# Performance work log

Hardware: AMD Instinct MI355X
Metric: run time of the kernel (lower is better)

The kernel has to match this reference:

```python
import jax, jax.numpy as jnp
import numpy as np

N_AUTHOR, N_PAPER = 20000, 40000
E = 400000
IN_DIM, HIDDEN, HEADS, NUM_CLASSES, NUM_LAYERS = 128, 128, 8, 16, 2
DIM = HIDDEN // HEADS
NEG_SLOPE = 0.2
AUTHOR_RAW = 64


def setup_inputs() -> dict:
    key = jax.random.key(0)
    ks = jax.random.split(key, 16)
    s = 0.05
    return {
        'x_author': jax.random.normal(ks[0], (N_AUTHOR, AUTHOR_RAW), jnp.float32),
        'x_paper': jax.random.normal(ks[1], (N_PAPER, IN_DIM), jnp.float32),
        'Wa': jax.random.normal(ks[2], (AUTHOR_RAW, IN_DIM), jnp.float32) * s,
        'proj_w': jax.random.normal(ks[3], (NUM_LAYERS, 2, IN_DIM, HIDDEN), jnp.float32) * s,
        'proj_b': jnp.zeros((NUM_LAYERS, 2, HIDDEN), jnp.float32),
        'att_src': jax.random.normal(ks[4], (NUM_LAYERS, 3, HEADS, DIM), jnp.float32) * s,
        'att_dst': jax.random.normal(ks[5], (NUM_LAYERS, 3, HEADS, DIM), jnp.float32) * s,
        'klin_w': jax.random.normal(ks[6], (NUM_LAYERS, HIDDEN, HIDDEN), jnp.float32) * s,
        'klin_b': jnp.zeros((NUM_LAYERS, HIDDEN), jnp.float32),
        'q': jax.random.normal(ks[7], (NUM_LAYERS, HIDDEN), jnp.float32) * s,
        'lin_w': jax.random.normal(ks[8], (HIDDEN, NUM_CLASSES), jnp.float32) * s,
        'lin_b': jnp.zeros((NUM_CLASSES,), jnp.float32),
        'ei_writes': jnp.stack([jax.random.randint(ks[9], (E,), 0, N_AUTHOR),
                                jax.random.randint(ks[10], (E,), 0, N_PAPER)]),
        'ei_written_by': jnp.stack([jax.random.randint(ks[11], (E,), 0, N_PAPER),
                                    jax.random.randint(ks[12], (E,), 0, N_AUTHOR)]),
        'ei_cites': jnp.stack([jax.random.randint(ks[13], (E,), 0, N_PAPER),
                               jax.random.randint(ks[14], (E,), 0, N_PAPER)]),
    }


def _segment_softmax(scores, seg, num_segments):
    # scores: [E, H]; softmax over edges sharing a destination node.
    m = jax.ops.segment_max(scores, seg, num_segments=num_segments)
    m = jnp.where(jnp.isfinite(m), m, 0.0)
    e = jnp.exp(scores - m[seg])
    denom = jax.ops.segment_sum(e, seg, num_segments=num_segments)
    return e / (denom[seg] + 1e-16)


def _han_forward(x_author, x_paper, Wa, proj_w, proj_b, att_src, att_dst,
                 klin_w, klin_b, q, lin_w, lin_b,
                 ei_writes, ei_written_by, ei_cites):
    # Type-alignment projector (author: 64 -> 128, no bias; paper: Identity)
    x = {'author': x_author @ Wa, 'paper': x_paper}
    nsize = {'author': N_AUTHOR, 'paper': N_PAPER}
    ntidx = {'author': 0, 'paper': 1}
    edge_types = [('author', 'paper', ei_writes),
                  ('paper', 'author', ei_written_by),
                  ('paper', 'paper', ei_cites)]
    for l in range(NUM_LAYERS):
        # Per-node-type projection -> [N, H, D]
        xh = {nt: (x[nt] @ proj_w[l, ntidx[nt]] + proj_b[l, ntidx[nt]]).reshape(-1, HEADS, DIM)
              for nt in x}
        outs = {'author': [], 'paper': []}
        for e_id, (src, dst, ei) in enumerate(edge_types):
            a_src = (xh[src] * att_src[l, e_id]).sum(-1)  # [N_src, H]
            a_dst = (xh[dst] * att_dst[l, e_id]).sum(-1)  # [N_dst, H]
            si, di = ei[0], ei[1]
            alpha = a_src[si] + a_dst[di]                 # [E, H]
            alpha = jnp.where(alpha >= 0, alpha, NEG_SLOPE * alpha)  # leaky_relu
            alpha = _segment_softmax(alpha, di, nsize[dst])
            # attention dropout omitted (eval mode)
            msg = (xh[src][si] * alpha[:, :, None]).reshape(-1, HIDDEN)  # [E, HIDDEN]
            agg = jax.ops.segment_sum(msg, di, num_segments=nsize[dst])
            outs[dst].append(jax.nn.relu(agg))
        # Semantic-level attention over metapath embeddings per node type
        newx = {}
        for nt, xs in outs.items():
            stk = jnp.stack(xs)  # [M, N, F]
            score = (q[l] * jnp.tanh(stk @ klin_w[l] + klin_b[l]).mean(axis=1)).sum(-1)  # [M]
            attn = jax.nn.softmax(score)
            newx[nt] = (attn[:, None, None] * stk).sum(0)
        x = newx
        if l < NUM_LAYERS - 1:
            x = {nt: jax.nn.relu(v) for nt, v in x.items()}
            # feature dropout omitted (eval mode)
    return x['paper'] @ lin_w + lin_b  # [N_PAPER, NUM_CLASSES]


def reference(x_author, x_paper, Wa, proj_w, proj_b, att_src, att_dst,
              klin_w, klin_b, q, lin_w, lin_b,
              ei_writes, ei_written_by, ei_cites):
    return _han_forward(x_author, x_paper, Wa, proj_w, proj_b, att_src, att_dst,
                        klin_w, klin_b, q, lin_w, lin_b,
                        ei_writes, ei_written_by, ei_cites)
```

## Files before the change

### kernel.cpp

```cpp
#include <hip/hip_runtime.h>
#include <hip/hip_bf16.h>

typedef __hip_bfloat16 bf16;
typedef __hip_bfloat162 bf162;

#define N_AUTHOR 20000
#define N_PAPER  40000
#define NEDGE    400000
#define HID      128
#define HEADS    8
#define DIMH     16
#define NCLS     16

typedef short short8v __attribute__((ext_vector_type(8)));
typedef float f32x4   __attribute__((ext_vector_type(4)));

__device__ __forceinline__ float b2f(short s){
    return __uint_as_float(((unsigned)(unsigned short)s) << 16);
}
__device__ __forceinline__ short f2bs(float v){
    unsigned u = __float_as_uint(v);
    unsigned r = (u + 0x7FFFu + ((u >> 16) & 1u)) >> 16;
    return (short)r;
}
__device__ __forceinline__ float fastrcp(float x){ return __builtin_amdgcn_rcpf(x); }

__device__ __forceinline__ float fast_tanh(float x){
    x = fminf(fmaxf(x, -15.f), 15.f);
    float e = __expf(2.f * x);
    return 1.f - 2.f * fastrcp(e + 1.f);
}

template<int KDIM, int EPI, int BLEND, int AF32>
__device__ __forceinline__ void bgemm_body(
    const void* __restrict__ Av, const bf16* __restrict__ A2, float w0, float w1,
    const bf16* __restrict__ Wt, const float* __restrict__ Bb,
    bf16* __restrict__ C, const float* __restrict__ qv, float* __restrict__ score,
    int M, int brow, float* red)
{
    const int tid  = threadIdx.x;
    const int lane = tid & 63;
    const int wv   = tid >> 6;
    const int lr   = lane & 15;
    const int quad = lane >> 4;
    const int row0 = brow * 64 + wv * 16;
    const int arow_i = row0 + lr;
    const bool rowok = arow_i < M;

    short8v afrag[KDIM / 32];
    if (AF32) {
        const float* arow = (const float*)Av + (long)arow_i * KDIM;
        #pragma unroll
        for (int kc = 0; kc < KDIM / 32; kc++) {
            short8v f = {0,0,0,0,0,0,0,0};
            if (rowok) {
                float4 v0 = *(const float4*)(arow + kc * 32 + quad * 8);
                float4 v1 = *(const float4*)(arow + kc * 32 + quad * 8 + 4);
                f[0] = f2bs(v0.x); f[1] = f2bs(v0.y); f[2] = f2bs(v0.z); f[3] = f2bs(v0.w);
                f[4] = f2bs(v1.x); f[5] = f2bs(v1.y); f[6] = f2bs(v1.z); f[7] = f2bs(v1.w);
            }
            afrag[kc] = f;
        }
    } else {
        const bf16* arow  = (const bf16*)Av + (long)arow_i * KDIM;
        const bf16* arow2 = BLEND ? (A2 + (long)arow_i * KDIM) : nullptr;
        #pragma unroll
        for (int kc = 0; kc < KDIM / 32; kc++) {
            short8v f = {0,0,0,0,0,0,0,0};
            if (rowok) {
                f = *(const short8v*)(arow + kc * 32 + quad * 8);
                if (BLEND) {
                    short8v g = *(const short8v*)(arow2 + kc * 32 + quad * 8);
                    #pragma unroll
                    for (int j = 0; j < 8; j++)
                        f[j] = f2bs(w0 * b2f(f[j]) + w1 * b2f(g[j]));
                }
            }
            afrag[kc] = f;
        }
    }

    f32x4 acc[8];
    #pragma unroll
    for (int ct = 0; ct < 8; ct++) acc[ct] = (f32x4){0.f, 0.f, 0.f, 0.f};

    #pragma unroll
    for (int k0 = 0; k0 < KDIM / 32; k0 += 2) {
        short8v bf[2][8];
        #pragma unroll
        for (int u = 0; u < 2; u++)
            #pragma unroll
            for (int ct = 0; ct < 8; ct++)
                bf[u][ct] = *(const short8v*)(Wt + (long)(ct * 16 + lr) * KDIM + (k0 + u) * 32 + quad * 8);
        #pragma unroll
        for (int u = 0; u < 2; u++)
            #pragma unroll
            for (int ct = 0; ct < 8; ct++)
                acc[ct] = __builtin_amdgcn_mfma_f32_16x16x32_bf16(afrag[k0 + u], bf[u][ct], acc[ct], 0, 0, 0);
    }

    if (EPI == 0) {
        #pragma unroll
        for (int ct = 0; ct < 8; ct++) {
            float bc = Bb ? Bb[ct * 16 + lr] : 0.f;
            #pragma unroll
            for (int r = 0; r < 4; r++) {
                int orow = row0 + quad * 4 + r;
                if (orow < M)
                    C[(long)orow * HID + ct * 16 + lr] = __float2bfloat16(acc[ct][r] + bc);
            }
        }
    } else {
        float part = 0.f;
        #pragma unroll
        for (int ct = 0; ct < 8; ct++) {
            float bc = Bb ? Bb[ct * 16 + lr] : 0.f;
            float qc = qv[ct * 16 + lr];
            #pragma unroll
            for (int r = 0; r < 4; r++) {
                int orow = row0 + quad * 4 + r;
                if (orow < M) part += qc * fast_tanh(acc[ct][r] + bc);
            }
        }
        red[tid] = part;
        __syncthreads();
        for (int s = 128; s > 0; s >>= 1) {
            if (tid < s) red[tid] += red[tid + s];
            __syncthreads();
        }
        if (tid == 0) atomicAdd(score, red[0]);
    }
}

template<int KDIM, int EPI, int B1>
__global__ __launch_bounds__(256) void bgemm_pair_kernel(
    const bf16* __restrict__ A0, const bf16* __restrict__ Wt0, const float* __restrict__ Bb0,
    bf16* __restrict__ C0, float* __restrict__ score0, int M0, int NB0,
    const bf16* __restrict__ A1, const bf16* __restrict__ A1b, const float* __restrict__ scw,
    const bf16* __restrict__ Wt1, const float* __restrict__ Bb1,
    bf16* __restrict__ C1, float* __restrict__ score1, int M1,
    const float* __restrict__ qv)
{
    __shared__ float red[256];
    const int bx = blockIdx.x;
    if (bx < NB0) {
        bgemm_body<KDIM, EPI, 0, 0>(A0, nullptr, 0.f, 0.f, Wt0, Bb0, C0, qv, score0, M0, bx, red);
    } else {
        float w0 = 0.f, w1 = 0.f;
        if (B1) {
            float s0 = scw[0] * (1.f / N_PAPER);
            float s1 = scw[1] * (1.f / N_PAPER);
            float m = fmaxf(s0, s1);
            float e0 = __expf(s0 - m), e1 = __expf(s1 - m);
            float inv = fastrcp(e0 + e1);
            w0 = e0 * inv; w1 = e1 * inv;
        }
        bgemm_body<KDIM, EPI, B1, 0>(A1, A1b, w0, w1, Wt1, Bb1, C1, qv, score1, M1, bx - NB0, red);
    }
}

#define R_WA  (128 * 64)
#define R_PW  (4 * 128 * 128)
#define R_KW  (2 * 128 * 128)
#define CONV_W_TOT (R_WA + R_PW + R_KW)

#define CNT_OFF1 N_PAPER
#define CNT_OFF2 (N_PAPER + N_AUTHOR)
#define NDEST    (2 * N_PAPER + N_AUTHOR)
#define NCOPY 8
#define CW    2
#define CIDX(c, d) (((c) * NDEST + (d)) * CW)
#define CNT_TOT (NCOPY * NDEST * CW)
#define E3 (3 * NEDGE)
#define HU 16
#define HIST_TT (E3 / HU)

__global__ __launch_bounds__(256) void convw_kernel(
    const float* __restrict__ Wa, const float* __restrict__ proj_w,
    const float* __restrict__ klin_w,
    bf16* __restrict__ wt_wa, bf16* __restrict__ wt_proj, bf16* __restrict__ wt_klin)
{
    int i = blockIdx.x * 256 + threadIdx.x;
    if (i >= CONV_W_TOT) return;
    if (i < R_WA) {
        int n = i >> 6, k = i & 63;
        wt_wa[i] = __float2bfloat16(Wa[k * 128 + n]);
    } else if (i < R_WA + R_PW) {
        int j = i - R_WA;
        int m = j >> 14, r = j & 16383;
        int n = r >> 7, k = r & 127;
        wt_proj[j] = __float2bfloat16(proj_w[m * 16384 + k * 128 + n]);
    } else {
        int j = i - R_WA - R_PW;
        int m = j >> 14, r = j & 16383;
        int n = r >> 7, k = r & 127;
        wt_klin[j] = __float2bfloat16(klin_w[m * 16384 + k * 128 + n]);
    }
}

__global__ __launch_bounds__(256) void hist_gemm_kernel(
    const int* __restrict__ d0, const int* __restrict__ d1, const int* __restrict__ d2,
    int* __restrict__ cnt, unsigned short* __restrict__ rank, int HB,
    const float* __restrict__ xa_f, const bf16* __restrict__ wt_wa, bf16* __restrict__ buf_a, int GA64,
    const float* __restrict__ xp_f, const bf16* __restrict__ pw_p, const float* __restrict__ pb_p,
    bf16* __restrict__ xh_p)
{
    __shared__ float red[256];
    int bx = blockIdx.x;
    if (bx < HB) {
        int c = bx & (NCOPY - 1);
        int* mycnt = cnt + c * NDEST * CW;
        int t = bx * 256 + threadIdx.x;
        if (t >= HIST_TT) return;
        #pragma unroll
        for (int u = 0; u < HU; u++) {
            int i = t + u * HIST_TT;
            int r;
            if (i < NEDGE)            r = atomicAdd(&mycnt[d0[i] * CW], 1);
            else if (i < 2*NEDGE)     r = atomicAdd(&mycnt[(CNT_OFF1 + d1[i - NEDGE]) * CW], 1);
            else                      r = atomicAdd(&mycnt[(CNT_OFF2 + d2[i - 2*NEDGE]) * CW], 1);
            rank[i] = (unsigned short)((c << 13) | r);
        }
        return;
    }
    bx -= HB;
    if (bx < GA64) {
        bgemm_body<64, 0, 0, 1>(xa_f, nullptr, 0.f, 0.f, wt_wa, nullptr, buf_a,
                                nullptr, nullptr, N_AUTHOR, bx, red);
        return;
    }
    bx -= GA64;
    bgemm_body<128, 0, 0, 1>(xp_f, nullptr, 0.f, 0.f, pw_p, pb_p, xh_p,
                             nullptr, nullptr, N_PAPER, bx, red);
}

__device__ __forceinline__ int job_nd(int j){ return j == 1 ? N_AUTHOR : N_PAPER; }
__device__ __forceinline__ int job_off(int j){ return j == 0 ? 0 : (j == 1 ? CNT_OFF1 : CNT_OFF2); }

__global__ __launch_bounds__(256) void scan_a3_kernel(const int* __restrict__ cnt,
                                                      int* __restrict__ bsum)
{
    int j = blockIdx.y;
    int nd = job_nd(j), off = job_off(j);
    __shared__ int s[256];
    int tid = threadIdx.x;
    int i = blockIdx.x * 256 + tid;
    int v = 0;
    if (i < nd) {
        #pragma unroll
        for (int c = 0; c < NCOPY; c++) v += cnt[CIDX(c, off + i)];
    }
    s[tid] = v;
    __syncthreads();
    for (int st = 128; st > 0; st >>= 1) {
        if (tid < st) s[tid] += s[tid + st];
        __syncthreads();
    }
    if (tid == 0) bsum[j * 256 + blockIdx.x] = s[0];
}

__global__ __launch_bounds__(256) void scan_bc_kernel(int* __restrict__ cnt,
    const int* __restrict__ bsum,
    int* __restrict__ roff0, int* __restrict__ roff1, int* __restrict__ roff2)
{
    int j = blockIdx.y;
    int nd = job_nd(j), off = job_off(j);
    int* roff = j == 0 ? roff0 : (j == 1 ? roff1 : roff2);
    __shared__ int sb[256];
    __shared__ int s[256];
    int tid = threadIdx.x;
    int bx = blockIdx.x;
    int nb = (nd + 255) / 256;
    int bvt = (tid < nb) ? bsum[j * 256 + tid] : 0;
    sb[tid] = bvt;
    __syncthreads();
    for (int o = 1; o < 256; o <<= 1) {
        int t = (tid >= o) ? sb[tid - o] : 0;
        __syncthreads();
        sb[tid] += t;
        __syncthreads();
    }
    int base0 = sb[bx] - bsum[j * 256 + bx];
    int i = bx * 256 + tid;
    int cc[NCOPY];
    int v = 0;
    if (i < nd) {
        #pragma unroll
        for (int c = 0; c < NCOPY; c++) { cc[c] = cnt[CIDX(c, off + i)]; v += cc[c]; }
    }
    s[tid] = v;
    __syncthreads();
    for (int o = 1; o < 256; o <<= 1) {
        int t = (tid >= o) ? s[tid - o] : 0;
        __syncthreads();
        s[tid] += t;
        __syncthreads();
    }
    if (i < nd) {
        int base = base0 + s[tid] - v;
        roff[i] = base;
        #pragma unroll
        for (int c = 0; c < NCOPY; c++) { cnt[CIDX(c, off + i)] = base; base += cc[c]; }
    }
    if (bx == 0 && tid == 0) roff[nd] = NEDGE;
}

__global__ __launch_bounds__(256) void fill_natt_kernel(
    const int* __restrict__ s0, const int* __restrict__ d0,
    const int* __restrict__ s1, const int* __restrict__ d1,
    const int* __restrict__ s2, const int* __restrict__ d2,
    const int* __restrict__ cnt, const unsigned short* __restrict__ rank,
    unsigned short* __restrict__ c0, unsigned short* __restrict__ c1, unsigned short* __restrict__ c2,
    int HB,
    const bf16* __restrict__ A, const bf16* __restrict__ Wt, const float* __restrict__ Bb,
    bf16* __restrict__ C, int GAb,
    const bf16* __restrict__ xh_p,
    const float* __restrict__ ad0v, const float* __restrict__ as1v,
    const float* __restrict__ as2v, const float* __restrict__ ad2v,
    float* __restrict__ o_e0d, float* __restrict__ o_e1s,
    float* __restrict__ o_e2s, float* __restrict__ o_e2d)
{
    __shared__ float red[256];
    int bx = blockIdx.x;
    if (bx < HB) {
        int t = bx * 256 + threadIdx.x;
        if (t >= HIST_TT) return;
        #pragma unroll
        for (int u = 0; u < HU; u++) {
            int i = t + u * HIST_TT;
            int rw = rank[i];
            int c = rw >> 13, rk = rw & 0x1FFF;
            if (i < NEDGE) {
                int d = d0[i];
                c0[cnt[CIDX(c, d)] + rk] = (unsigned short)s0[i];
            } else if (i < 2*NEDGE) {
                int e = i - NEDGE, d = d1[e];
                c1[cnt[CIDX(c, CNT_OFF1 + d)] + rk] = (unsigned short)s1[e];
            } else {
                int e = i - 2*NEDGE, d = d2[e];
                c2[cnt[CIDX(c, CNT_OFF2 + d)] + rk] = (unsigned short)s2[e];
            }
        }
        return;
    }
    bx -= HB;
    if (bx < GAb) {
        bgemm_body<128, 0, 0, 0>(A, nullptr, 0.f, 0.f, Wt, Bb, C,
                                 nullptr, nullptr, N_AUTHOR, bx, red);
        return;
    }
    bx -= GAb;
    int i = bx * 256 + threadIdx.x;
    if (i >= N_PAPER * HEADS) return;
    int n = i >> 3, h = i & 7;
    const bf16* row = xh_p + (long)n * HID + h * DIMH;
    float x[DIMH];
    #pragma unroll
    for (int d = 0; d < DIMH; d++) x[d] = __bfloat162float(row[d]);
    float sA = 0.f, sB = 0.f, sC = 0.f, sD = 0.f;
    #pragma unroll
    for (int d = 0; d < DIMH; d++) {
        sA += x[d] * ad0v[h*DIMH + d];
        sB += x[d] * as1v[h*DIMH + d];
        sC += x[d] * as2v[h*DIMH + d];
        sD += x[d] * ad2v[h*DIMH + d];
    }
    o_e0d[i] = sA; o_e1s[i] = sB; o_e2s[i] = sC; o_e2d[i] = sD;
}

__global__ void node_att_multi_kernel(const bf16* __restrict__ xh,
    const float* __restrict__ A0, const float* __restrict__ A1,
    float* __restrict__ O0, float* __restrict__ O1, int N)
{
    int i = blockIdx.x * blockDim.x + threadIdx.x;
    if (i >= N * HEADS) return;
    int n = i >> 3, h = i & 7;
    const bf16* row = xh + (long)n * HID + h * DIMH;
    float x[DIMH];
    #pragma unroll
    for (int d = 0; d < DIMH; d++) x[d] = __bfloat162float(row[d]);
    if (A0) { float s = 0.f;
        #pragma unroll
        for (int d = 0; d < DIMH; d++) s += x[d] * A0[h*DIMH + d];
        O0[i] = s; }
    if (A1) { float s = 0.f;
        #pragma unroll
        for (int d = 0; d < DIMH; d++) s += x[d] * A1[h*DIMH + d];
        O1[i] = s; }
}

__global__ __launch_bounds__(256) void natt_l1_kernel(
    const bf16* __restrict__ xh_a, const float* __restrict__ as0, float* __restrict__ a_e0s, int AB,
    const bf16* __restrict__ xh_p, const float* __restrict__ ad0,
    const float* __restrict__ as2, const float* __restrict__ ad2,
    float* __restrict__ a_e0d, float* __restrict__ a_e2s, float* __restrict__ a_e2d)
{
    int bx = blockIdx.x, tid = threadIdx.x;
    if (bx < AB) {
        int i = bx * 256 + tid;
        if (i >= N_AUTHOR * HEADS) return;
        int n = i >> 3, h = i & 7;
        const bf16* row = xh_a + (long)n * HID + h * DIMH;
        float s = 0.f;
        #pragma unroll
        for (int d = 0; d < DIMH; d++) s += __bfloat162float(row[d]) * as0[h*DIMH + d];
        a_e0s[i] = s;
        return;
    }
    int i = (bx - AB) * 256 + tid;
    if (i >= N_PAPER * HEADS) return;
    int n = i >> 3, h = i & 7;
    const bf16* row = xh_p + (long)n * HID + h * DIMH;
    float x[DIMH];
    #pragma unroll
    for (int d = 0; d < DIMH; d++) x[d] = __bfloat162float(row[d]);
    float sA = 0.f, sC = 0.f, sD = 0.f;
    #pragma unroll
    for (int d = 0; d < DIMH; d++) {
        sA += x[d] * ad0[h*DIMH + d];
        sC += x[d] * as2[h*DIMH + d];
        sD += x[d] * ad2[h*DIMH + d];
    }
    a_e0d[i] = sA; a_e2s[i] = sC; a_e2d[i] = sD;
}

template<int U>
__device__ __forceinline__ void gather1_dev(int bid,
    const int* __restrict__ roff, const unsigned short* __restrict__ csrc,
    const float* __restrict__ as_, const float* __restrict__ ad_,
    const bf16* __restrict__ xh, bf16* __restrict__ out, int Ndst)
{
    int lane = threadIdx.x & 63;
    int li   = lane & 15;
    int sub  = lane >> 4;
    int w = bid * 16 + (threadIdx.x >> 6) * 4 + sub;
    if (w >= Ndst) return;
    int h = li >> 1;
    int beg = roff[w], n = roff[w + 1] - beg;
    float adv = ad_[(long)w * 8 + h];
    float den = 0.f;
    float acc[8];
    #pragma unroll
    for (int j = 0; j < 8; j++) acc[j] = 0.f;
    int cm = n > 0 ? n - 1 : 0;
    for (int i = 0; i < n; i += U) {
        int s[U];
        #pragma unroll
        for (int u = 0; u < U; u++) s[u] = csrc[beg + min(i + u, cm)];
        float av[U]; short8v xv[U];
        #pragma unroll
        for (int u = 0; u < U; u++) {
            av[u] = as_[(long)s[u] * 8 + h];
            xv[u] = *(const short8v*)(xh + (long)s[u] * HID + li * 8);
        }
        #pragma unroll
        for (int u = 0; u < U; u++) {
            float a = av[u] + adv;
            a = a >= 0.f ? a : 0.2f * a;
            float wt = __expf(fminf(a, 60.f));
            wt = (i + u < n) ? wt : 0.f;
            den += wt;
            #pragma unroll
            for (int j = 0; j < 8; j++)
                acc[j] = fmaf(b2f(xv[u][j]), wt, acc[j]);
        }
    }
    float inv = fastrcp(den + 1e-16f);
    short8v o;
    #pragma unroll
    for (int j = 0; j < 8; j++) o[j] = f2bs(fmaxf(acc[j] * inv, 0.f));
    *(short8v*)(out + (long)w * HID + li * 8) = o;
}

__global__ __launch_bounds__(256) void gather_split_kernel(
    const int* __restrict__ roff0, const unsigned short* __restrict__ csrc0,
    const float* __restrict__ as0, const float* __restrict__ ad0,
    const bf16* __restrict__ xha, bf16* __restrict__ out0,
    const int* __restrict__ roff2, const unsigned short* __restrict__ csrc2,
    const float* __restrict__ as2, const float* __restrict__ ad2,
    const bf16* __restrict__ xhp, bf16* __restrict__ out2,
    int PB,
    const int* __restrict__ roff1, const unsigned short* __restrict__ csrc1,
    const float* __restrict__ as1, const float* __restrict__ ad1,
    bf16* __restrict__ out_a)
{
    int bx = blockIdx.x;
    if (bx < PB) {
        gather1_dev<8>(bx, roff0, csrc0, as0, ad0, xha, out0, N_PAPER);
        return;
    }
    bx -= PB;
    if (bx < PB) {
        gather1_dev<8>(bx, roff2, csrc2, as2, ad2, xhp, out2, N_PAPER);
        return;
    }
    bx -= PB;
    gather1_dev<8>(bx, roff1, csrc1, as1, ad1, xhp, out_a, N_AUTHOR);
}

__global__ __launch_bounds__(256) void final_lin_fused_kernel(
    const bf16* __restrict__ a0, const bf16* __restrict__ a1,
    const float* __restrict__ score,
    const float* __restrict__ W, const float* __restrict__ B, float* __restrict__ out)
{
    __shared__ float Ws[HID * NCLS];
    int tid = threadIdx.x;
    for (int i = tid; i < HID * NCLS; i += 256) Ws[i] = W[i];
    __syncthreads();
    float s0 = score[0] * (1.f / N_PAPER);
    float s1 = score[1] * (1.f / N_PAPER);
    float m = fmaxf(s0, s1);
    float e0 = __expf(s0 - m), e1 = __expf(s1 - m);
    float inv = 1.f / (e0 + e1);
    float w0 = e0 * inv, w1 = e1 * inv;
    int i = blockIdx.x * 256 + tid;
    if (i >= N_PAPER * NCLS) return;
    int n = i >> 4, c = i & 15;
    float acc = B[c];
    const bf16* x0 = a0 + (long)n * HID;
    const bf16* x1 = a1 + (long)n * HID;
    #pragma unroll 16
    for (int k = 0; k < HID; k++)
        acc = fmaf(fmaf(w0, __bfloat162float(x0[k]), w1 * __bfloat162float(x1[k])),
                   Ws[k * NCLS + c], acc);
    out[i] = acc;
}

extern "C" void kernel_launch(void* const* d_in, const int* in_sizes, int n_in,
                              void* d_out, int out_size, void* d_ws, size_t ws_size,
                              hipStream_t stream)
{
    const float* x_author = (const float*)d_in[0];
    const float* x_paper  = (const float*)d_in[1];
    const float* Wa       = (const float*)d_in[2];
    const float* proj_w   = (const float*)d_in[3];
    const float* proj_b   = (const float*)d_in[4];
    const float* att_src  = (const float*)d_in[5];
    const float* att_dst  = (const float*)d_in[6];
    const float* klin_w   = (const float*)d_in[7];
    const float* klin_b   = (const float*)d_in[8];
    const float* qv       = (const float*)d_in[9];
    const float* lin_w    = (const float*)d_in[10];
    const float* lin_b    = (const float*)d_in[11];
    const int*  ei_w      = (const int*)d_in[12];
    const int*  ei_wb     = (const int*)d_in[13];
    const int*  ei_c      = (const int*)d_in[14];
    float* out = (float*)d_out;
    (void)ws_size; (void)in_sizes; (void)n_in; (void)out_size;

    char* base = (char*)d_ws;
    size_t off = 0;
    auto alloc = [&](size_t bytes) {
        void* p = base + off;
        off = (off + bytes + 255) & ~(size_t)255;
        return p;
    };
    bf16*  xh_a  = (bf16*) alloc((size_t)N_AUTHOR * HID * 2);
    bf16*  xh_p  = (bf16*) alloc((size_t)N_PAPER  * HID * 2);
    bf16*  buf_a = (bf16*) alloc((size_t)N_AUTHOR * HID * 2);
    bf16*  buf_p = (bf16*) alloc((size_t)N_PAPER  * HID * 2);
    bf16*  agg_p1= (bf16*) alloc((size_t)N_PAPER  * HID * 2);
    bf16*  wt_wa   = (bf16*)alloc((size_t)R_WA * 2);
    bf16*  wt_proj = (bf16*)alloc((size_t)R_PW * 2);
    bf16*  wt_klin = (bf16*)alloc((size_t)R_KW * 2);
    float* a_e0s = (float*)alloc((size_t)N_AUTHOR * HEADS * 4);
    float* a_e0d = (float*)alloc((size_t)N_PAPER  * HEADS * 4);
    float* a_e1s = (float*)alloc((size_t)N_PAPER  * HEADS * 4);
    float* a_e1d = (float*)alloc((size_t)N_AUTHOR * HEADS * 4);
    float* a_e2s = (float*)alloc((size_t)N_PAPER  * HEADS * 4);
    float* a_e2d = (float*)alloc((size_t)N_PAPER  * HEADS * 4);
    float* score  = (float*)alloc(64);
    int* roff0 = (int*)alloc((size_t)(N_PAPER  + 1) * 4);
    int* roff1 = (int*)alloc((size_t)(N_AUTHOR + 1) * 4);
    int* roff2 = (int*)alloc((size_t)(N_PAPER  + 1) * 4);
    unsigned short* csrc0 = (unsigned short*)alloc((size_t)NEDGE * 2 + 64);
    unsigned short* csrc1 = (unsigned short*)alloc((size_t)NEDGE * 2 + 64);
    unsigned short* csrc2 = (unsigned short*)alloc((size_t)NEDGE * 2 + 64);
    int* cnt   = (int*)alloc((size_t)CNT_TOT * 4);
    unsigned short* rank = (unsigned short*)alloc((size_t)E3 * 2);
    int* bsum  = (int*)alloc(3 * 256 * 4);

    const int GA = (N_AUTHOR + 63) / 64;
    const int GP = (N_PAPER  + 63) / 64;
    const int NBMAX = (N_PAPER + 255) / 256;
    const int HB = (HIST_TT + 255) / 256;
    const int CONVB = (CONV_W_TOT + 255) / 256;
    const int NATTP = (N_PAPER * HEADS + 255) / 256;
    const int NATTA = (N_AUTHOR * HEADS + 255) / 256;
    const int PGB = (N_PAPER + 15) / 16;
    const int AGB = (N_AUTHOR + 15) / 16;

    hipMemsetAsync(cnt, 0, (size_t)CNT_TOT * 4, stream);
    hipMemsetAsync(score, 0, 64, stream);

    convw_kernel<<<CONVB, 256, 0, stream>>>(
        Wa, proj_w, klin_w, wt_wa, wt_proj, wt_klin);
    hist_gemm_kernel<<<HB + GA + GP, 256, 0, stream>>>(
        ei_w + NEDGE, ei_wb + NEDGE, ei_c + NEDGE, cnt, rank, HB,
        x_author, wt_wa, buf_a, GA,
        x_paper, wt_proj + (size_t)1 * HID * HID, proj_b + (size_t)1 * HID, xh_p);
    scan_a3_kernel<<<dim3(NBMAX, 3), 256, 0, stream>>>(cnt, bsum);
    scan_bc_kernel<<<dim3(NBMAX, 3), 256, 0, stream>>>(cnt, bsum, roff0, roff1, roff2);

    const float* as0_0 = att_src + 0 * HID; const float* ad0_0 = att_dst + 0 * HID;
    const float* as1_0 = att_src + 1 * HID; const float* ad1_0 = att_dst + 1 * HID;
    const float* as2_0 = att_src + 2 * HID; const float* ad2_0 = att_dst + 2 * HID;

    fill_natt_kernel<<<HB + GA + NATTP, 256, 0, stream>>>(
        ei_w, ei_w + NEDGE, ei_wb, ei_wb + NEDGE, ei_c, ei_c + NEDGE,
        cnt, rank, csrc0, csrc1, csrc2, HB,
        buf_a, wt_proj + (size_t)0 * HID * HID, proj_b + (size_t)0 * HID, xh_a, GA,
        xh_p, ad0_0, as1_0, as2_0, ad2_0,
        a_e0d, a_e1s, a_e2s, a_e2d);
    node_att_multi_kernel<<<NATTA, 256, 0, stream>>>(
        xh_a, as0_0, ad1_0, a_e0s, a_e1d, N_AUTHOR);

    gather_split_kernel<<<2 * PGB + AGB, 256, 0, stream>>>(
        roff0, csrc0, a_e0s, a_e0d, xh_a, buf_p,
        roff2, csrc2, a_e2s, a_e2d, xh_p, agg_p1,
        PGB,
        roff1, csrc1, a_e1s, a_e1d, buf_a);

    bgemm_pair_kernel<128, 1, 0><<<2 * GP, 256, 0, stream>>>(
        buf_p, wt_klin, klin_b, (bf16*)nullptr, score + 0, N_PAPER, GP,
        agg_p1, nullptr, nullptr, wt_klin, klin_b, (bf16*)nullptr, score + 1, N_PAPER,
        qv);

    bgemm_pair_kernel<128, 0, 1><<<GA + GP, 256, 0, stream>>>(
        buf_a, wt_proj + (size_t)2 * HID * HID, proj_b + (size_t)2 * HID, xh_a,
        nullptr, N_AUTHOR, GA,
        buf_p, agg_p1, score,
        wt_proj + (size_t)3 * HID * HID, proj_b + (size_t)3 * HID, xh_p,
        nullptr, N_PAPER, nullptr);
    hipMemsetAsync(score, 0, 64, stream);

    const float* as0_1 = att_src + 3 * HID; const float* ad0_1 = att_dst + 3 * HID;
    const float* as2_1 = att_src + 5 * HID; const float* ad2_1 = att_dst + 5 * HID;

    natt_l1_kernel<<<NATTA + NATTP, 256, 0, stream>>>(
        xh_a, as0_1, a_e0s, NATTA,
        xh_p, ad0_1, as2_1, ad2_1, a_e0d, a_e2s, a_e2d);

    gather_split_kernel<<<2 * PGB, 256, 0, stream>>>(
        roff0, csrc0, a_e0s, a_e0d, xh_a, buf_p,
        roff2, csrc2, a_e2s, a_e2d, xh_p, agg_p1,
        PGB,
        roff1, csrc1, a_e1s, a_e1d, nullptr);

    bgemm_pair_kernel<128, 1, 0><<<2 * GP, 256, 0, stream>>>(
        buf_p, wt_klin + (size_t)HID * HID, klin_b + HID, (bf16*)nullptr, score + 0, N_PAPER, GP,
        agg_p1, nullptr, nullptr, wt_klin + (size_t)HID * HID, klin_b + HID,
        (bf16*)nullptr, score + 1, N_PAPER,
        qv + HID);

    final_lin_fused_kernel<<<(N_PAPER * NCLS + 255) / 256, 256, 0, stream>>>(
        buf_p, agg_p1, score, lin_w, lin_b, out);
}
```

Baseline: 397.1 us.

## Replace global atomic histogram with LDS-partitioned per-copy histograms

The destination-count histogram now runs in shared memory. Each block owns one of 8 edge chunks and one 8192-wide destination range, scans the whole chunk, does LDS atomics for in-range destinations, then writes its counts to global memory. This removes the global atomics, the padded count stride and the memset of the count array. In exchange, each edge index is read 13 times across the partitions, the block count is fixed at 104 per histogram, and the GEMM blocks share a larger 32 KB LDS allocation, which may reduce their occupancy.

```diff
diff --git a/kernel.cpp b/kernel.cpp
--- a/kernel.cpp
+++ b/kernel.cpp
@@ -168,12 +168,16 @@
 #define CNT_OFF2 (N_PAPER + N_AUTHOR)
 #define NDEST    (2 * N_PAPER + N_AUTHOR)
 #define NCOPY 8
-#define CW    2
-#define CIDX(c, d) (((c) * NDEST + (d)) * CW)
-#define CNT_TOT (NCOPY * NDEST * CW)
+#define CIDX(c, d) ((c) * NDEST + (d))
+#define CNT_TOT (NCOPY * NDEST)
 #define E3 (3 * NEDGE)
 #define HU 16
 #define HIST_TT (E3 / HU)
+
+#define PART_SZ 8192
+#define NPART   13
+#define CHUNK   (E3 / NCOPY)
+#define HBLK    (NPART * NCOPY)
 
 __global__ __launch_bounds__(256) void convw_kernel(
     const float* __restrict__ Wa, const float* __restrict__ proj_w,
@@ -200,38 +204,61 @@
 
 __global__ __launch_bounds__(256) void hist_gemm_kernel(
     const int* __restrict__ d0, const int* __restrict__ d1, const int* __restrict__ d2,
-    int* __restrict__ cnt, unsigned short* __restrict__ rank, int HB,
+    int* __restrict__ cnt, unsigned short* __restrict__ rank,
     const float* __restrict__ xa_f, const bf16* __restrict__ wt_wa, bf16* __restrict__ buf_a, int GA64,
     const float* __restrict__ xp_f, const bf16* __restrict__ pw_p, const float* __restrict__ pb_p,
     bf16* __restrict__ xh_p)
 {
-    __shared__ float red[256];
+    __shared__ int lh[PART_SZ];
     int bx = blockIdx.x;
-    if (bx < HB) {
-        int c = bx & (NCOPY - 1);
-        int* mycnt = cnt + c * NDEST * CW;
-        int t = bx * 256 + threadIdx.x;
-        if (t >= HIST_TT) return;
-        #pragma unroll
-        for (int u = 0; u < HU; u++) {
-            int i = t + u * HIST_TT;
-            int r;
-            if (i < NEDGE)            r = atomicAdd(&mycnt[d0[i] * CW], 1);
-            else if (i < 2*NEDGE)     r = atomicAdd(&mycnt[(CNT_OFF1 + d1[i - NEDGE]) * CW], 1);
-            else                      r = atomicAdd(&mycnt[(CNT_OFF2 + d2[i - 2*NEDGE]) * CW], 1);
-            rank[i] = (unsigned short)((c << 13) | r);
+    int tid = threadIdx.x;
+    if (bx < HBLK) {
+        int p = bx % NPART;
+        int c = bx / NPART;
+        #pragma unroll
+        for (int k = tid; k < PART_SZ; k += 256) lh[k] = 0;
+        __syncthreads();
+        const int base = c * CHUNK;
+        const int lo = p * PART_SZ;
+        for (int k0 = 0; k0 < CHUNK; k0 += 2048) {
+            int dd[8];
+            #pragma unroll
+            for (int u = 0; u < 8; u++) {
+                int k = k0 + u * 256 + tid;
+                int dglob = -1;
+                if (k < CHUNK) {
+                    int i = base + k;
+                    if (i < NEDGE)          dglob = d0[i];
+                    else if (i < 2*NEDGE)   dglob = CNT_OFF1 + d1[i - NEDGE];
+                    else                    dglob = CNT_OFF2 + d2[i - 2*NEDGE];
+                }
+                dd[u] = dglob;
+            }
+            #pragma unroll
+            for (int u = 0; u < 8; u++) {
+                int ld = dd[u] - lo;
+                if (dd[u] >= 0 && ld >= 0 && ld < PART_SZ) {
+                    int r = atomicAdd(&lh[ld], 1);
+                    rank[base + k0 + u * 256 + tid] = (unsigned short)((c << 13) | r);
+                }
+            }
+        }
+        __syncthreads();
+        for (int ld = tid; ld < PART_SZ; ld += 256) {
+            int d = lo + ld;
+            if (d < NDEST) cnt[CIDX(c, d)] = lh[ld];
         }
         return;
     }
-    bx -= HB;
+    bx -= HBLK;
     if (bx < GA64) {
         bgemm_body<64, 0, 0, 1>(xa_f, nullptr, 0.f, 0.f, wt_wa, nullptr, buf_a,
-                                nullptr, nullptr, N_AUTHOR, bx, red);
+                                nullptr, nullptr, N_AUTHOR, bx, (float*)lh);
         return;
     }
     bx -= GA64;
     bgemm_body<128, 0, 0, 1>(xp_f, nullptr, 0.f, 0.f, pw_p, pb_p, xh_p,
-                             nullptr, nullptr, N_PAPER, bx, red);
+                             nullptr, nullptr, N_PAPER, bx, (float*)lh);
 }
 
 __device__ __forceinline__ int job_nd(int j){ return j == 1 ? N_AUTHOR : N_PAPER; }
@@ -590,13 +617,12 @@
     const int PGB = (N_PAPER + 15) / 16;
     const int AGB = (N_AUTHOR + 15) / 16;
 
-    hipMemsetAsync(cnt, 0, (size_t)CNT_TOT * 4, stream);
     hipMemsetAsync(score, 0, 64, stream);
 
     convw_kernel<<<CONVB, 256, 0, stream>>>(
         Wa, proj_w, klin_w, wt_wa, wt_proj, wt_klin);
-    hist_gemm_kernel<<<HB + GA + GP, 256, 0, stream>>>(
-        ei_w + NEDGE, ei_wb + NEDGE, ei_c + NEDGE, cnt, rank, HB,
+    hist_gemm_kernel<<<HBLK + GA + GP, 256, 0, stream>>>(
+        ei_w + NEDGE, ei_wb + NEDGE, ei_c + NEDGE, cnt, rank,
         x_author, wt_wa, buf_a, GA,
         x_paper, wt_proj + (size_t)1 * HID * HID, proj_b + (size_t)1 * HID, xh_p);
     scan_a3_kernel<<<dim3(NBMAX, 3), 256, 0, stream>>>(cnt, bsum);
```

Measured after the change: 573.2 us. +44.3%, slower.

## Fuse node attention dot products into projection GEMM epilogues and regroup launches

Applied to the files above, without the earlier changes.

Computes the per-head attention source/destination scores directly in the projection GEMM epilogue from the fp32 accumulators, using cross-lane shuffles over 16 columns. This removes the separate node-attention kernels, which re-read the bf16 projected features. Launches are regrouped: the author projection for layer 1 now runs alongside the semantic klin GEMMs in one mid kernel, and the paper projection gets its own kernel. The trade-off is extra shuffle work and scattered 4-byte stores in the GEMM epilogue, and the attention scores now come from unrounded fp32 values rather than bf16.

```diff
diff --git a/kernel.cpp b/kernel.cpp
--- a/kernel.cpp
+++ b/kernel.cpp
@@ -31,12 +31,16 @@
     return 1.f - 2.f * fastrcp(e + 1.f);
 }
 
-template<int KDIM, int EPI, int BLEND, int AF32>
+template<int KDIM, int EPI, int BLEND, int AF32, int NATT>
 __device__ __forceinline__ void bgemm_body(
     const void* __restrict__ Av, const bf16* __restrict__ A2, float w0, float w1,
     const bf16* __restrict__ Wt, const float* __restrict__ Bb,
     bf16* __restrict__ C, const float* __restrict__ qv, float* __restrict__ score,
-    int M, int brow, float* red)
+    int M, int brow, float* red,
+    const float* __restrict__ at0, const float* __restrict__ at1,
+    const float* __restrict__ at2, const float* __restrict__ at3,
+    float* __restrict__ o0, float* __restrict__ o1,
+    float* __restrict__ o2, float* __restrict__ o3)
 {
     const int tid  = threadIdx.x;
     const int lane = tid & 63;
@@ -103,11 +107,35 @@
         #pragma unroll
         for (int ct = 0; ct < 8; ct++) {
             float bc = Bb ? Bb[ct * 16 + lr] : 0.f;
+            float av0 = (NATT > 0) ? at0[ct * 16 + lr] : 0.f;
+            float av1 = (NATT > 1) ? at1[ct * 16 + lr] : 0.f;
+            float av2 = (NATT > 2) ? at2[ct * 16 + lr] : 0.f;
+            float av3 = (NATT > 3) ? at3[ct * 16 + lr] : 0.f;
             #pragma unroll
             for (int r = 0; r < 4; r++) {
                 int orow = row0 + quad * 4 + r;
+                float cb = acc[ct][r] + bc;
                 if (orow < M)
-                    C[(long)orow * HID + ct * 16 + lr] = __float2bfloat16(acc[ct][r] + bc);
+                    C[(long)orow * HID + ct * 16 + lr] = __float2bfloat16(cb);
+                if (NATT > 0) {
+                    float d0 = cb * av0;
+                    float d1 = cb * av1;
+                    float d2 = cb * av2;
+                    float d3 = cb * av3;
+                    #pragma unroll
+                    for (int mm = 1; mm < 16; mm <<= 1) {
+                        d0 += __shfl_xor(d0, mm);
+                        if (NATT > 1) d1 += __shfl_xor(d1, mm);
+                        if (NATT > 2) d2 += __shfl_xor(d2, mm);
+                        if (NATT > 3) d3 += __shfl_xor(d3, mm);
+                    }
+                    if (lr == 0 && orow < M) {
+                        o0[(long)orow * 8 + ct] = d0;
+                        if (NATT > 1) o1[(long)orow * 8 + ct] = d1;
+                        if (NATT > 2) o2[(long)orow * 8 + ct] = d2;
+                        if (NATT > 3) o3[(long)orow * 8 + ct] = d3;
+                    }
+                }
             }
         }
     } else {
@@ -129,33 +157,6 @@
             __syncthreads();
         }
         if (tid == 0) atomicAdd(score, red[0]);
-    }
-}
-
-template<int KDIM, int EPI, int B1>
-__global__ __launch_bounds__(256) void bgemm_pair_kernel(
-    const bf16* __restrict__ A0, const bf16* __restrict__ Wt0, const float* __restrict__ Bb0,
-    bf16* __restrict__ C0, float* __restrict__ score0, int M0, int NB0,
-    const bf16* __restrict__ A1, const bf16* __restrict__ A1b, const float* __restrict__ scw,
-    const bf16* __restrict__ Wt1, const float* __restrict__ Bb1,
-    bf16* __restrict__ C1, float* __restrict__ score1, int M1,
-    const float* __restrict__ qv)
-{
-    __shared__ float red[256];
-    const int bx = blockIdx.x;
-    if (bx < NB0) {
-        bgemm_body<KDIM, EPI, 0, 0>(A0, nullptr, 0.f, 0.f, Wt0, Bb0, C0, qv, score0, M0, bx, red);
-    } else {
-        float w0 = 0.f, w1 = 0.f;
-        if (B1) {
-            float s0 = scw[0] * (1.f / N_PAPER);
-            float s1 = scw[1] * (1.f / N_PAPER);
-            float m = fmaxf(s0, s1);
-            float e0 = __expf(s0 - m), e1 = __expf(s1 - m);
-            float inv = fastrcp(e0 + e1);
-            w0 = e0 * inv; w1 = e1 * inv;
-        }
-        bgemm_body<KDIM, EPI, B1, 0>(A1, A1b, w0, w1, Wt1, Bb1, C1, qv, score1, M1, bx - NB0, red);
     }
 }
 
@@ -203,7 +204,11 @@
     int* __restrict__ cnt, unsigned short* __restrict__ rank, int HB,
     const float* __restrict__ xa_f, const bf16* __restrict__ wt_wa, bf16* __restrict__ buf_a, int GA64,
     const float* __restrict__ xp_f, const bf16* __restrict__ pw_p, const float* __restrict__ pb_p,
-    bf16* __restrict__ xh_p)
+    bf16* __restrict__ xh_p,
+    const float* __restrict__ ad0v, const float* __restrict__ as1v,
+    const float* __restrict__ as2v, const float* __restrict__ ad2v,
+    float* __restrict__ a_e0d, float* __restrict__ a_e1s,
+    float* __restrict__ a_e2s, float* __restrict__ a_e2d)
 {
     __shared__ float red[256];
     int bx = blockIdx.x;
@@ -225,13 +230,17 @@
     }
     bx -= HB;
     if (bx < GA64) {
-        bgemm_body<64, 0, 0, 1>(xa_f, nullptr, 0.f, 0.f, wt_wa, nullptr, buf_a,
-                                nullptr, nullptr, N_AUTHOR, bx, red);
+        bgemm_body<64, 0, 0, 1, 0>(xa_f, nullptr, 0.f, 0.f, wt_wa, nullptr, buf_a,
+                                   nullptr, nullptr, N_AUTHOR, bx, red,
+                                   nullptr, nullptr, nullptr, nullptr,
+                                   nullptr, nullptr, nullptr, nullptr);
         return;
     }
     bx -= GA64;
-    bgemm_body<128, 0, 0, 1>(xp_f, nullptr, 0.f, 0.f, pw_p, pb_p, xh_p,
-                             nullptr, nullptr, N_PAPER, bx, red);
+    bgemm_body<128, 0, 0, 1, 4>(xp_f, nullptr, 0.f, 0.f, pw_p, pb_p, xh_p,
+                                nullptr, nullptr, N_PAPER, bx, red,
+                                ad0v, as1v, as2v, ad2v,
+                                a_e0d, a_e1s, a_e2s, a_e2d);
 }
 
 __device__ __forceinline__ int job_nd(int j){ return j == 1 ? N_AUTHOR : N_PAPER; }
@@ -305,7 +314,7 @@
     if (bx == 0 && tid == 0) roff[nd] = NEDGE;
 }
 
-__global__ __launch_bounds__(256) void fill_natt_kernel(
+__global__ __launch_bounds__(256) void fill_gemm_kernel(
     const int* __restrict__ s0, const int* __restrict__ d0,
     const int* __restrict__ s1, const int* __restrict__ d1,
     const int* __restrict__ s2, const int* __restrict__ d2,
@@ -313,12 +322,9 @@
     unsigned short* __restrict__ c0, unsigned short* __restrict__ c1, unsigned short* __restrict__ c2,
     int HB,
     const bf16* __restrict__ A, const bf16* __restrict__ Wt, const float* __restrict__ Bb,
-    bf16* __restrict__ C, int GAb,
-    const bf16* __restrict__ xh_p,
-    const float* __restrict__ ad0v, const float* __restrict__ as1v,
-    const float* __restrict__ as2v, const float* __restrict__ ad2v,
-    float* __restrict__ o_e0d, float* __restrict__ o_e1s,
-    float* __restrict__ o_e2s, float* __restrict__ o_e2d)
+    bf16* __restrict__ C,
+    const float* __restrict__ as0v, const float* __restrict__ ad1v,
+    float* __restrict__ a_e0s, float* __restrict__ a_e1d)
 {
     __shared__ float red[256];
     int bx = blockIdx.x;
@@ -344,84 +350,82 @@
         return;
     }
     bx -= HB;
-    if (bx < GAb) {
-        bgemm_body<128, 0, 0, 0>(A, nullptr, 0.f, 0.f, Wt, Bb, C,
-                                 nullptr, nullptr, N_AUTHOR, bx, red);
+    bgemm_body<128, 0, 0, 0, 2>(A, nullptr, 0.f, 0.f, Wt, Bb, C,
+                                nullptr, nullptr, N_AUTHOR, bx, red,
+                                as0v, ad1v, nullptr, nullptr,
+                                a_e0s, a_e1d, nullptr, nullptr);
+}
+
+__global__ __launch_bounds__(256) void mid_kernel(
+    const bf16* __restrict__ buf_p, const bf16* __restrict__ agg_p1,
+    const bf16* __restrict__ kw, const float* __restrict__ kb,
+    float* __restrict__ score, const float* __restrict__ qq, int GP_,
+    const bf16* __restrict__ buf_a, const bf16* __restrict__ pw_a, const float* __restrict__ pb_a,
+    bf16* __restrict__ xh_a,
+    const float* __restrict__ as0v, float* __restrict__ a_e0s)
+{
+    __shared__ float red[256];
+    int bx = blockIdx.x;
+    if (bx < GP_) {
+        bgemm_body<128, 1, 0, 0, 0>(buf_p, nullptr, 0.f, 0.f, kw, kb, nullptr,
+                                    qq, score + 0, N_PAPER, bx, red,
+                                    nullptr, nullptr, nullptr, nullptr,
+                                    nullptr, nullptr, nullptr, nullptr);
         return;
     }
-    bx -= GAb;
-    int i = bx * 256 + threadIdx.x;
-    if (i >= N_PAPER * HEADS) return;
-    int n = i >> 3, h = i & 7;
-    const bf16* row = xh_p + (long)n * HID + h * DIMH;
-    float x[DIMH];
-    #pragma unroll
-    for (int d = 0; d < DIMH; d++) x[d] = __bfloat162float(row[d]);
-    float sA = 0.f, sB = 0.f, sC = 0.f, sD = 0.f;
-    #pragma unroll
-    for (int d = 0; d < DIMH; d++) {
-        sA += x[d] * ad0v[h*DIMH + d];
-        sB += x[d] * as1v[h*DIMH + d];
-        sC += x[d] * as2v[h*DIMH + d];
-        sD += x[d] * ad2v[h*DIMH + d];
-    }
-    o_e0d[i] = sA; o_e1s[i] = sB; o_e2s[i] = sC; o_e2d[i] = sD;
-}
-
-__global__ void node_att_multi_kernel(const bf16* __restrict__ xh,
-    const float* __restrict__ A0, const float* __restrict__ A1,
-    float* __restrict__ O0, float* __restrict__ O1, int N)
-{
-    int i = blockIdx.x * blockDim.x + threadIdx.x;
-    if (i >= N * HEADS) return;
-    int n = i >> 3, h = i & 7;
-    const bf16* row = xh + (long)n * HID + h * DIMH;
-    float x[DIMH];
-    #pragma unroll
-    for (int d = 0; d < DIMH; d++) x[d] = __bfloat162float(row[d]);
-    if (A0) { float s = 0.f;
-        #pragma unroll
-        for (int d = 0; d < DIMH; d++) s += x[d] * A0[h*DIMH + d];
-        O0[i] = s; }
-    if (A1) { float s = 0.f;
-        #pragma unroll
-        for (int d = 0; d < DIMH; d++) s += x[d] * A1[h*DIMH + d];
-        O1[i] = s; }
-}
-
-__global__ __launch_bounds__(256) void natt_l1_kernel(
-    const bf16* __restrict__ xh_a, const float* __restrict__ as0, float* __restrict__ a_e0s, int AB,
-    const bf16* __restrict__ xh_p, const float* __restrict__ ad0,
-    const float* __restrict__ as2, const float* __restrict__ ad2,
+    bx -= GP_;
+    if (bx < GP_) {
+        bgemm_body<128, 1, 0, 0, 0>(agg_p1, nullptr, 0.f, 0.f, kw, kb, nullptr,
+                                    qq, score + 1, N_PAPER, bx, red,
+                                    nullptr, nullptr, nullptr, nullptr,
+                                    nullptr, nullptr, nullptr, nullptr);
+        return;
+    }
+    bx -= GP_;
+    bgemm_body<128, 0, 0, 0, 1>(buf_a, nullptr, 0.f, 0.f, pw_a, pb_a, xh_a,
+                                nullptr, nullptr, N_AUTHOR, bx, red,
+                                as0v, nullptr, nullptr, nullptr,
+                                a_e0s, nullptr, nullptr, nullptr);
+}
+
+__global__ __launch_bounds__(256) void pproj_kernel(
+    const bf16* __restrict__ buf_p, const bf16* __restrict__ agg_p1,
+    const float* __restrict__ scw,
+    const bf16* __restrict__ pw_p, const float* __restrict__ pb_p,
+    bf16* __restrict__ xh_p,
+    const float* __restrict__ ad0v, const float* __restrict__ as2v, const float* __restrict__ ad2v,
     float* __restrict__ a_e0d, float* __restrict__ a_e2s, float* __restrict__ a_e2d)
 {
-    int bx = blockIdx.x, tid = threadIdx.x;
-    if (bx < AB) {
-        int i = bx * 256 + tid;
-        if (i >= N_AUTHOR * HEADS) return;
-        int n = i >> 3, h = i & 7;
-        const bf16* row = xh_a + (long)n * HID + h * DIMH;
-        float s = 0.f;
-        #pragma unroll
-        for (int d = 0; d < DIMH; d++) s += __bfloat162float(row[d]) * as0[h*DIMH + d];
-        a_e0s[i] = s;
-        return;
-    }
-    int i = (bx - AB) * 256 + tid;
-    if (i >= N_PAPER * HEADS) return;
-    int n = i >> 3, h = i & 7;
-    const bf16* row = xh_p + (long)n * HID + h * DIMH;
-    float x[DIMH];
-    #pragma unroll
-    for (int d = 0; d < DIMH; d++) x[d] = __bfloat162float(row[d]);
-    float sA = 0.f, sC = 0.f, sD = 0.f;
-    #pragma unroll
-    for (int d = 0; d < DIMH; d++) {
-        sA += x[d] * ad0[h*DIMH + d];
-        sC += x[d] * as2[h*DIMH + d];
-        sD += x[d] * ad2[h*DIMH + d];
-    }
-    a_e0d[i] = sA; a_e2s[i] = sC; a_e2d[i] = sD;
+    __shared__ float red[256];
+    float s0 = scw[0] * (1.f / N_PAPER);
+    float s1 = scw[1] * (1.f / N_PAPER);
+    float m = fmaxf(s0, s1);
+    float e0 = __expf(s0 - m), e1 = __expf(s1 - m);
+    float inv = fastrcp(e0 + e1);
+    float w0 = e0 * inv, w1 = e1 * inv;
+    bgemm_body<128, 0, 1, 0, 3>(buf_p, agg_p1, w0, w1, pw_p, pb_p, xh_p,
+                                nullptr, nullptr, N_PAPER, blockIdx.x, red,
+                                ad0v, as2v, ad2v, nullptr,
+                                a_e0d, a_e2s, a_e2d, nullptr);
+}
+
+__global__ __launch_bounds__(256) void klin_pair_kernel(
+    const bf16* __restrict__ A0, const bf16* __restrict__ A1,
+    const bf16* __restrict__ kw, const float* __restrict__ kb,
+    float* __restrict__ score, const float* __restrict__ qq, int GP_)
+{
+    __shared__ float red[256];
+    int bx = blockIdx.x;
+    if (bx < GP_)
+        bgemm_body<128, 1, 0, 0, 0>(A0, nullptr, 0.f, 0.f, kw, kb, nullptr,
+                                    qq, score + 0, N_PAPER, bx, red,
+                                    nullptr, nullptr, nullptr, nullptr,
+                                    nullptr, nullptr, nullptr, nullptr);
+    else
+        bgemm_body<128, 1, 0, 0, 0>(A1, nullptr, 0.f, 0.f, kw, kb, nullptr,
+                                    qq, score + 1, N_PAPER, bx - GP_, red,
+                                    nullptr, nullptr, nullptr, nullptr,
+                                    nullptr, nullptr, nullptr, nullptr);
 }
 
 template<int U>
@@ -585,10 +589,14 @@
     const int NBMAX = (N_PAPER + 255) / 256;
     const int HB = (HIST_TT + 255) / 256;
     const int CONVB = (CONV_W_TOT + 255) / 256;
-    const int NATTP = (N_PAPER * HEADS + 255) / 256;
-    const int NATTA = (N_AUTHOR * HEADS + 255) / 256;
     const int PGB = (N_PAPER + 15) / 16;
     const int AGB = (N_AUTHOR + 15) / 16;
+
+    const float* as0_0 = att_src + 0 * HID; const float* ad0_0 = att_dst + 0 * HID;
+    const float* as1_0 = att_src + 1 * HID; const float* ad1_0 = att_dst + 1 * HID;
+    const float* as2_0 = att_src + 2 * HID; const float* ad2_0 = att_dst + 2 * HID;
+    const float* as0_1 = att_src + 3 * HID; const float* ad0_1 = att_dst + 3 * HID;
+    const float* as2_1 = att_src + 5 * HID; const float* ad2_1 = att_dst + 5 * HID;
 
     hipMemsetAsync(cnt, 0, (size_t)CNT_TOT * 4, stream);
     hipMemsetAsync(score, 0, 64, stream);
@@ -598,22 +606,17 @@
     hist_gemm_kernel<<<HB + GA + GP, 256, 0, stream>>>(
         ei_w + NEDGE, ei_wb + NEDGE, ei_c + NEDGE, cnt, rank, HB,
         x_author, wt_wa, buf_a, GA,
-        x_paper, wt_proj + (size_t)1 * HID * HID, proj_b + (size_t)1 * HID, xh_p);
+        x_paper, wt_proj + (size_t)1 * HID * HID, proj_b + (size_t)1 * HID, xh_p,
+        ad0_0, as1_0, as2_0, ad2_0,
+        a_e0d, a_e1s, a_e2s, a_e2d);
     scan_a3_kernel<<<dim3(NBMAX, 3), 256, 0, stream>>>(cnt, bsum);
     scan_bc_kernel<<<dim3(NBMAX, 3), 256, 0, stream>>>(cnt, bsum, roff0, roff1, roff2);
 
-    const float* as0_0 = att_src + 0 * HID; const float* ad0_0 = att_dst + 0 * HID;
-    const float* as1_0 = att_src + 1 * HID; const float* ad1_0 = att_dst + 1 * HID;
-    const float* as2_0 = att_src + 2 * HID; const float* ad2_0 = att_dst + 2 * HID;
-
-    fill_natt_kernel<<<HB + GA + NATTP, 256, 0, stream>>>(
+    fill_gemm_kernel<<<HB + GA, 256, 0, stream>>>(
         ei_w, ei_w + NEDGE, ei_wb, ei_wb + NEDGE, ei_c, ei_c + NEDGE,
         cnt, rank, csrc0, csrc1, csrc2, HB,
-        buf_a, wt_proj + (size_t)0 * HID * HID, proj_b + (size_t)0 * HID, xh_a, GA,
-        xh_p, ad0_0, as1_0, as2_0, ad2_0,
-        a_e0d, a_e1s, a_e2s, a_e2d);
-    node_att_multi_kernel<<<NATTA, 256, 0, stream>>>(
-        xh_a, as0_0, ad1_0, a_e0s, a_e1d, N_AUTHOR);
+        buf_a, wt_proj + (size_t)0 * HID * HID, proj_b + (size_t)0 * HID, xh_a,
+        as0_0, ad1_0, a_e0s, a_e1d);
 
     gather_split_kernel<<<2 * PGB + AGB, 256, 0, stream>>>(
         roff0, csrc0, a_e0s, a_e0d, xh_a, buf_p,
@@ -621,25 +624,16 @@
         PGB,
         roff1, csrc1, a_e1s, a_e1d, buf_a);
 
-    bgemm_pair_kernel<128, 1, 0><<<2 * GP, 256, 0, stream>>>(
-        buf_p, wt_klin, klin_b, (bf16*)nullptr, score + 0, N_PAPER, GP,
-        agg_p1, nullptr, nullptr, wt_klin, klin_b, (bf16*)nullptr, score + 1, N_PAPER,
-        qv);
-
-    bgemm_pair_kernel<128, 0, 1><<<GA + GP, 256, 0, stream>>>(
+    mid_kernel<<<2 * GP + GA, 256, 0, stream>>>(
+        buf_p, agg_p1, wt_klin, klin_b, score, qv, GP,
         buf_a, wt_proj + (size_t)2 * HID * HID, proj_b + (size_t)2 * HID, xh_a,
-        nullptr, N_AUTHOR, GA,
+        as0_1, a_e0s);
+
+    pproj_kernel<<<GP, 256, 0, stream>>>(
         buf_p, agg_p1, score,
         wt_proj + (size_t)3 * HID * HID, proj_b + (size_t)3 * HID, xh_p,
-        nullptr, N_PAPER, nullptr);
+        ad0_1, as2_1, ad2_1, a_e0d, a_e2s, a_e2d);
     hipMemsetAsync(score, 0, 64, stream);
-
-    const float* as0_1 = att_src + 3 * HID; const float* ad0_1 = att_dst + 3 * HID;
-    const float* as2_1 = att_src + 5 * HID; const float* ad2_1 = att_dst + 5 * HID;
-
-    natt_l1_kernel<<<NATTA + NATTP, 256, 0, stream>>>(
-        xh_a, as0_1, a_e0s, NATTA,
-        xh_p, ad0_1, as2_1, ad2_1, a_e0d, a_e2s, a_e2d);
 
     gather_split_kernel<<<2 * PGB, 256, 0, stream>>>(
         roff0, csrc0, a_e0s, a_e0d, xh_a, buf_p,
@@ -647,11 +641,9 @@
         PGB,
         roff1, csrc1, a_e1s, a_e1d, nullptr);
 
-    bgemm_pair_kernel<128, 1, 0><<<2 * GP, 256, 0, stream>>>(
-        buf_p, wt_klin + (size_t)HID * HID, klin_b + HID, (bf16*)nullptr, score + 0, N_PAPER, GP,
-        agg_p1, nullptr, nullptr, wt_klin + (size_t)HID * HID, klin_b + HID,
-        (bf16*)nullptr, score + 1, N_PAPER,
-        qv + HID);
+    klin_pair_kernel<<<2 * GP, 256, 0, stream>>>(
+        buf_p, agg_p1, wt_klin + (size_t)HID * HID, klin_b + HID,
+        score, qv + HID, GP);
 
     final_lin_fused_kernel<<<(N_PAPER * NCLS + 255) / 256, 256, 0, stream>>>(
         buf_p, agg_p1, score, lin_w, lin_b, out);
```

Measured after the change: 411.4 us. 1.04x slower.
